# Optimization experiments

Measured on AMD Instinct MI355X. Metric: run time of the kernel, lower is better.

The kernel has to match this reference:

```python
import jax, jax.numpy as jnp
import numpy as np

EMB = 300; H = 150; DEC = 300
VU = 50000; VQ = 30000; VS = 5000
N_COLS = 64; COL_LEN = 6; N_TURNS = 6; IN_LEN = 128; GEN_LEN = 64
MAX_KEEP = 5


def _lstm_cell(x, h, c, Wih, Whh, b):
    z = x @ Wih.T + h @ Whh.T + b
    i, f, g, o = jnp.split(z, 4)
    c = jax.nn.sigmoid(f) * c + jax.nn.sigmoid(i) * jnp.tanh(g)
    h = jax.nn.sigmoid(o) * jnp.tanh(c)
    return h, c


def _run_lstm(xs, Wih, Whh, b):
    hsz = Whh.shape[-1]
    z = jnp.zeros((hsz,), xs.dtype)
    def step(carry, x):
        h, c = _lstm_cell(x, carry[0], carry[1], Wih, Whh, b)
        return (h, c), h
    (h, c), ys = jax.lax.scan(step, (z, z), xs)
    return ys, h, c


def _bilstm(xs, Wih, Whh, b):
    # Wih: [2, 4H, in], Whh: [2, 4H, H], b: [2, 4H]
    yf, hf, cf = _run_lstm(xs, Wih[0], Whh[0], b[0])
    yb, hb, cb = _run_lstm(xs[::-1], Wih[1], Whh[1], b[1])
    return jnp.concatenate([yf, yb[::-1]], -1), jnp.concatenate([hf, hb], -1), jnp.concatenate([cf, cb], -1)


def _attention(q, keys, Wq, Wk, v):
    # Bahdanau: v^T tanh(Wq q + Wk k); context = softmax-weighted sum of keys
    s = jnp.tanh(q @ Wq + keys @ Wk) @ v
    return jax.nn.softmax(s) @ keys


def _forward(utter_emb, query_emb, schema_tok_emb, enc_Wih, enc_Whh, enc_b,
             attn_Wq, attn_Wk, attn_v, dec_Wih0, dec_Whh0, dec_b0,
             dec_Wih1, dec_Whh1, dec_b1, transform_W, sql_W, sql_b, col_W,
             schema_tokens, input_seqs, output_gt):
    attn = lambda k_i, q, keys: _attention(q, keys, attn_Wq[k_i], attn_Wk[k_i], attn_v[k_i])
    # --- schema column encoding: BiLSTM over each column's name tokens ---
    col_tok = schema_tok_emb[schema_tokens]                       # [C, L, EMB]
    _, h, _ = jax.vmap(lambda xs: _bilstm(xs, enc_Wih[0], enc_Whh[0], enc_b[0]))(col_tok)
    schema_embs = h                                               # [C, EMB]
    prev_in, prev_h, prev_c, prev_out = [], [], [], []
    all_dists = []
    bos_emb = query_emb[0]
    for i in range(N_TURNS):
        idx = input_seqs[i]
        # mixed vocab / schema-pointer embedding lookup
        x = jnp.where((idx < VU)[:, None],
                      utter_emb[jnp.clip(idx, 0, VU - 1)],
                      schema_embs[jnp.clip(idx - VU, 0, N_COLS - 1)])
        x, _, _ = _bilstm(x, enc_Wih[1], enc_Whh[1], enc_b[1])    # utter_encoder
        # TextSchemaEncoder (approx): second BiLSTM + schema cross-attention update
        x, fh, fc = _bilstm(x, enc_Wih[2], enc_Whh[2], enc_b[2])
        schema_embs = schema_embs + jax.nn.softmax(schema_embs @ x.T, -1) @ x
        h0, c0 = fh, fc
        if i > 0:
            hist_h = jnp.stack(prev_h); hist_c = jnp.stack(prev_c)
            h0n = h0 + attn(0, h0, hist_h)
            c0 = h0n + attn(0, c0, hist_c)  # replicates original's h-based c init
            h0 = h0n
        prev_in = (prev_in + [x])[:MAX_KEEP]
        prev_h = (prev_h + [fh])[:MAX_KEEP]
        prev_c = (prev_c + [fc])[:MAX_KEEP]
        keys_in = jnp.concatenate(prev_in, 0)
        keys_out = jnp.concatenate(prev_out, 0) if i > 0 else None
        se = schema_embs

        def embed_out(t):
            return jnp.where(t < VQ,
                             query_emb[jnp.clip(t, 0, VQ - 1)],
                             se[jnp.clip(t - VQ, 0, N_COLS - 1)])

        def dec_step(carry, t):
            h1p, c1p, h2p, c2p, dh = carry
            out_emb = embed_out(t)  # teacher forcing
            ctx_s = attn(1, dh, se)
            ctx_i = attn(2, dh, keys_in)
            ctx_o = attn(3, dh, keys_out) if keys_out is not None else jnp.zeros_like(ctx_i)
            ctx = jnp.concatenate([ctx_s, ctx_i, ctx_o])
            xin = jnp.concatenate([out_emb, ctx])                 # [4*EMB]
            h1, c1 = _lstm_cell(xin, h1p, c1p, dec_Wih0, dec_Whh0, dec_b0)
            h2, c2 = _lstm_cell(h1, h2p, c2p, dec_Wih1, dec_Whh1, dec_b1)
            out = jnp.tanh(jnp.concatenate([h2, ctx]) @ transform_W.T)
            score = jnp.concatenate([out @ sql_W.T + sql_b, (out @ col_W.T) @ se.T])
            dist = jax.nn.log_softmax(score)
            am_emb = embed_out(jnp.argmax(dist))
            return (h1, c1, h2, c2, h2), (dist, am_emb)

        init = (h0, c0, h0, c0, h0)
        _, (dists, am_embs) = jax.lax.scan(dec_step, init, output_gt[i, :GEN_LEN - 1])
        prev_out = (prev_out + [jnp.concatenate([bos_emb[None], am_embs], 0)])[:MAX_KEEP]
        all_dists.append(dists)
    return jnp.stack(all_dists, 0)  # [N_TURNS, GEN_LEN-1, VQ+N_COLS]


def setup_inputs() -> dict:
    key = jax.random.key(0)
    ks = jax.random.split(key, 24)
    s = 0.05
    f = lambda k, shape: jax.random.normal(k, shape, jnp.float32) * s
    return {
        "utter_emb": f(ks[0], (VU, EMB)),
        "query_emb": f(ks[1], (VQ, EMB)),
        "schema_tok_emb": f(ks[2], (VS, EMB)),
        "enc_Wih": f(ks[3], (3, 2, 4 * H, EMB)),   # [schema, utter, text-schema] x [fwd, bwd]
        "enc_Whh": f(ks[4], (3, 2, 4 * H, H)),
        "enc_b": f(ks[5], (3, 2, 4 * H)),
        "attn_Wq": f(ks[6], (4, EMB, EMB)),        # [turn, schema, in_tok, out_tok]
        "attn_Wk": f(ks[7], (4, EMB, EMB)),
        "attn_v": f(ks[8], (4, EMB)),
        "dec_Wih0": f(ks[9], (4 * DEC, 4 * EMB)),
        "dec_Whh0": f(ks[10], (4 * DEC, DEC)),
        "dec_b0": f(ks[11], (4 * DEC,)),
        "dec_Wih1": f(ks[12], (4 * DEC, DEC)),
        "dec_Whh1": f(ks[13], (4 * DEC, DEC)),
        "dec_b1": f(ks[14], (4 * DEC,)),
        "transform_W": f(ks[15], (EMB, 4 * EMB)),
        "sql_W": f(ks[16], (VQ, EMB)),
        "sql_b": f(ks[17], (VQ,)),
        "col_W": f(ks[18], (EMB, EMB)),
        "schema_tokens": jax.random.randint(ks[19], (N_COLS, COL_LEN), 0, VS),
        "input_seqs": jax.random.randint(ks[20], (N_TURNS, IN_LEN), 0, VU + N_COLS),
        "output_gt": jax.random.randint(ks[21], (N_TURNS, GEN_LEN), 0, VQ + N_COLS),
    }


def reference(utter_emb, query_emb, schema_tok_emb, enc_Wih, enc_Whh, enc_b,
              attn_Wq, attn_Wk, attn_v, dec_Wih0, dec_Whh0, dec_b0,
              dec_Wih1, dec_Whh1, dec_b1, transform_W, sql_W, sql_b, col_W,
              schema_tokens, input_seqs, output_gt):
    return _forward(utter_emb, query_emb, schema_tok_emb, enc_Wih, enc_Whh, enc_b,
                    attn_Wq, attn_Wk, attn_v, dec_Wih0, dec_Whh0, dec_b0,
                    dec_Wih1, dec_Whh1, dec_b1, transform_W, sql_W, sql_b, col_W,
                    schema_tokens, input_seqs, output_gt)
```

## Files before the change

### kernel.cpp

```cpp
#include <hip/hip_runtime.h>

#define EMB 300
#define VU 50000
#define VQ 30000
#define NCOLS 64
#define COLLEN 6
#define NTURNS 6
#define INLEN 128
#define TSTEPS 63
#define VOUT 30064
#define MAXK 5
#define NWD 60

__device__ __forceinline__ float sigf(float x){ return 1.0f/(1.0f+__expf(-x)); }
__device__ __forceinline__ float tanhf_(float x){ return 1.0f - 2.0f/(1.0f+__expf(2.0f*x)); }
__device__ __forceinline__ float wsum(float v){
#pragma unroll
  for (int o=32;o;o>>=1) v += __shfl_xor(v,o);
  return v;
}
__device__ __forceinline__ float wmax(float v){
#pragma unroll
  for (int o=32;o;o>>=1) v = fmaxf(v,__shfl_xor(v,o));
  return v;
}

__device__ __forceinline__ void gstore(float* p, float v){
  __hip_atomic_store((int*)p, __float_as_int(v), __ATOMIC_RELAXED, __HIP_MEMORY_SCOPE_AGENT);
}
__device__ __forceinline__ float gload(const float* p){
  return __int_as_float(__hip_atomic_load((const int*)p, __ATOMIC_RELAXED, __HIP_MEMORY_SCOPE_AGENT));
}

__device__ __forceinline__ void garrive(int* flags, int w, int P){
  asm volatile("s_waitcnt vmcnt(0)" ::: "memory");
  __syncthreads();
  if (threadIdx.x == 0)
    __hip_atomic_store(flags + w, P, __ATOMIC_RELAXED, __HIP_MEMORY_SCOPE_AGENT);
}
__device__ __forceinline__ void gwait(const int* flags, int P){
  if (threadIdx.x < 64) {
    int v;
    do {
      v = (threadIdx.x < NWD) ? __hip_atomic_load(flags + threadIdx.x, __ATOMIC_RELAXED, __HIP_MEMORY_SCOPE_AGENT) : P;
    } while (__any(v < P));
  }
  __syncthreads();
}

__global__ void k_init(int* flags){ if (threadIdx.x < 64) flags[threadIdx.x] = 0; }

__global__ void k_transposeB(const float* __restrict__ in, float* __restrict__ out,
                             int R, int C, size_t mstride)
{
  __shared__ float tile[32][33];
  const float* inp = in + (size_t)blockIdx.z*mstride;
  float* outp = out + (size_t)blockIdx.z*mstride;
  const int rb = blockIdx.y*32, cb = blockIdx.x*32;
  const int tx = threadIdx.x & 31, ty = threadIdx.x >> 5;
  for (int k = 0; k < 32; k += 8) {
    int r = rb + ty + k, c = cb + tx;
    if (r < R && c < C) tile[ty+k][tx] = inp[(size_t)r*C + c];
  }
  __syncthreads();
  for (int k = 0; k < 32; k += 8) {
    int c = cb + ty + k, r = rb + tx;
    if (c < C && r < R) outp[(size_t)c*R + r] = tile[tx][ty+k];
  }
}

__global__ void k_schema(const float* __restrict__ temb, const int* __restrict__ stok,
                         const float* __restrict__ Wih, const float* __restrict__ Whh,
                         const float* __restrict__ bb, float* __restrict__ SE0)
{
  const int col = blockIdx.x >> 1, dir = blockIdx.x & 1, tid = threadIdx.x;
  __shared__ float hl[150], cl[150], zl[600];
  if (tid < 150) { hl[tid]=0.f; cl[tid]=0.f; }
  __syncthreads();
  const float* Wi = Wih + (size_t)dir*600*300;
  const float* Wh = Whh + (size_t)dir*600*150;
  const float* bd = bb + dir*600;
  for (int s = 0; s < COLLEN; ++s) {
    const int pos = dir ? (COLLEN-1-s) : s;
    const int tok = stok[col*COLLEN + pos];
    const float* x = temb + (size_t)tok*300;
    for (int g = tid; g < 600; g += 256) {
      float a = bd[g];
      const float* wi = Wi + (size_t)g*300;
      for (int c = 0; c < 300; ++c) a += x[c]*wi[c];
      const float* wh = Wh + (size_t)g*150;
      for (int j = 0; j < 150; ++j) a += hl[j]*wh[j];
      zl[g] = a;
    }
    __syncthreads();
    if (tid < 150) {
      float ii=zl[tid], ff=zl[150+tid], gg=zl[300+tid], oo=zl[450+tid];
      float cn = sigf(ff)*cl[tid] + sigf(ii)*tanhf_(gg);
      cl[tid]=cn; hl[tid]=sigf(oo)*tanhf_(cn);
    }
    __syncthreads();
  }
  if (tid < 150) SE0[(size_t)col*300 + dir*150 + tid] = hl[tid];
}

__global__ void k_gemm_xe(const float* __restrict__ src, const float* __restrict__ SEi,
                          const int* __restrict__ iseq, int mode,
                          const float* __restrict__ WihL, const float* __restrict__ bL,
                          float* __restrict__ Xg)
{
  const int g = blockIdx.x*256 + threadIdx.x;
  if (g >= 1200) return;
  const int p0 = blockIdx.y*16;
  const float* xr[16];
#pragma unroll
  for (int t = 0; t < 16; ++t) {
    int p = p0 + t;
    if (mode) xr[t] = src + (size_t)p*300;
    else {
      int tok = iseq[p];
      xr[t] = (tok < VU) ? src + (size_t)tok*300 : SEi + (size_t)(tok - VU)*300;
    }
  }
  const float b = bL[g];
  const float* w = WihL + (size_t)g*300;
  float acc[16];
#pragma unroll
  for (int t = 0; t < 16; ++t) acc[t] = b;
  for (int c = 0; c < 300; ++c) {
    float wv = w[c];
#pragma unroll
    for (int t = 0; t < 16; ++t) acc[t] += wv * xr[t][c];
  }
#pragma unroll
  for (int t = 0; t < 16; ++t) Xg[(size_t)(p0+t)*1200 + g] = acc[t];
}

__global__ __launch_bounds__(640) void k_rec(
    const float* __restrict__ Xg, const float* __restrict__ WhhTL,
    float* __restrict__ ys, float* __restrict__ fh, float* __restrict__ fc)
{
  const int dir = blockIdx.x, tid = threadIdx.x;
  __shared__ __align__(16) float hl[152];
  __shared__ float cl[152], zl[600];
  float w[150];
  const float* wt = WhhTL + (size_t)dir*150*600;
  if (tid < 600) {
#pragma unroll
    for (int j = 0; j < 150; ++j) w[j] = wt[(size_t)j*600 + tid];
  }
  if (tid < 152) { hl[tid] = 0.f; cl[tid] = 0.f; }
  __syncthreads();
  for (int s = 0; s < INLEN; ++s) {
    const int pos = dir ? (INLEN-1-s) : s;
    if (tid < 600) {
      float acc = Xg[(size_t)pos*1200 + dir*600 + tid];
      const float4* h4 = (const float4*)hl;
#pragma unroll
      for (int j4 = 0; j4 < 37; ++j4) {
        float4 h = h4[j4];
        acc += w[4*j4]*h.x + w[4*j4+1]*h.y + w[4*j4+2]*h.z + w[4*j4+3]*h.w;
      }
      acc += w[148]*hl[148] + w[149]*hl[149];
      zl[tid] = acc;
    }
    __syncthreads();
    if (tid < 150) {
      float ii=zl[tid], ff=zl[150+tid], gg=zl[300+tid], oo=zl[450+tid];
      float cn = sigf(ff)*cl[tid] + sigf(ii)*tanhf_(gg);
      cl[tid] = cn;
      float hn = sigf(oo)*tanhf_(cn);
      hl[tid] = hn;
      ys[(size_t)pos*300 + dir*150 + tid] = hn;
    }
    __syncthreads();
  }
  if (tid < 150) { fh[dir*150 + tid] = hl[tid]; fc[dir*150 + tid] = cl[tid]; }
}

__global__ void k_schema_upd(const float* __restrict__ SEi, const float* __restrict__ ys2,
                             float* __restrict__ SEo)
{
  const int row = blockIdx.x, tid = threadIdx.x;
  __shared__ float sl[300], al[128], red[4];
  for (int d = tid; d < 300; d += 256) sl[d] = SEi[(size_t)row*300 + d];
  __syncthreads();
  if (tid < 128) {
    float a = 0;
    const float* yr = ys2 + (size_t)tid*300;
    for (int d = 0; d < 300; ++d) a += sl[d]*yr[d];
    al[tid] = a;
  }
  __syncthreads();
  if (tid < 64) { float m = fmaxf(al[tid], al[tid+64]); m = wmax(m); if (tid==0) red[0]=m; }
  __syncthreads();
  if (tid < 128) al[tid] = __expf(al[tid] - red[0]);
  __syncthreads();
  if (tid < 64) { float s = al[tid] + al[tid+64]; s = wsum(s); if (tid==0) red[1]=s; }
  __syncthreads();
  const float invz = 1.0f/red[1];
  for (int d = tid; d < 300; d += 256) {
    float a = sl[d];
    for (int j = 0; j < 128; ++j) a += (al[j]*invz) * ys2[(size_t)j*300 + d];
    SEo[(size_t)row*300 + d] = a;
  }
}

__global__ void k_hist(const float* __restrict__ fh, const float* __restrict__ fc,
                       const float* __restrict__ ys2,
                       float* __restrict__ HH, float* __restrict__ CH,
                       float* __restrict__ XH, int turn)
{
  const int tid = threadIdx.x;
  for (int i = blockIdx.x*256 + tid; i < INLEN*300; i += 60*256)
    XH[(size_t)turn*INLEN*300 + i] = ys2[i];
  if (blockIdx.x == 0)
    for (int d = tid; d < 300; d += 256) { HH[turn*300+d] = fh[d]; CH[turn*300+d] = fc[d]; }
}

__device__ __forceinline__ const float* key_ptr(int j, int nin, const float* SE1,
                                                const float* XH, const float* OH, int* fam)
{
  if (j < 64) { *fam = 0; return SE1 + (size_t)j*300; }
  if (j < 64+nin) { *fam = 1; return XH + (size_t)(j-64)*300; }
  *fam = 2; return OH + (size_t)(j-64-nin)*300;
}

__global__ void k_tables(const float* __restrict__ SE1, const float* __restrict__ XH,
                         const float* __restrict__ OH, const float* __restrict__ Wk,
                         const float* __restrict__ Wih0, const float* __restrict__ b0,
                         const float* __restrict__ tW, const float* __restrict__ qemb,
                         const int* __restrict__ gt,
                         float* __restrict__ KW, float* __restrict__ G1K,
                         float* __restrict__ G2K, float* __restrict__ Ew,
                         int nin, int nout)
{
  const int NK = 64 + nin + nout;
  const int b = blockIdx.x;
  if (b < NK) {
    int fam; const float* Kr = key_ptr(b, nin, SE1, XH, OH, &fam);
    const float* W = Wk + (size_t)(1+fam)*90000;
    for (int c = threadIdx.x; c < 300; c += 256) {
      float a = 0;
      for (int d = 0; d < 300; ++d) a += Kr[d]*W[(size_t)d*300 + c];
      KW[(size_t)b*300 + c] = a;
    }
  } else if (b < 2*NK) {
    int j = b - NK;
    int fam; const float* Kr = key_ptr(j, nin, SE1, XH, OH, &fam);
    const int cb = 300 + fam*300;
    for (int r = threadIdx.x; r < 1200; r += 256) {
      float a = 0;
      const float* wp = Wih0 + (size_t)r*1200 + cb;
      for (int c = 0; c < 300; ++c) a += Kr[c]*wp[c];
      G1K[(size_t)j*1200 + r] = a;
    }
  } else if (b < 3*NK) {
    int j = b - 2*NK;
    int fam; const float* Kr = key_ptr(j, nin, SE1, XH, OH, &fam);
    const int cb = 300 + fam*300;
    for (int r = threadIdx.x; r < 300; r += 256) {
      float a = 0;
      const float* wp = tW + (size_t)r*1200 + cb;
      for (int c = 0; c < 300; ++c) a += Kr[c]*wp[c];
      G2K[(size_t)j*300 + r] = a;
    }
  } else {
    int t = b - 3*NK;
    int tok = gt[t];
    const float* e = (tok < VQ) ? qemb + (size_t)tok*300 : SE1 + (size_t)(tok-VQ)*300;
    for (int r = threadIdx.x; r < 1200; r += 256) {
      float a = b0[r];
      const float* wp = Wih0 + (size_t)r*1200;
      for (int c = 0; c < 300; ++c) a += e[c]*wp[c];
      Ew[(size_t)t*1200 + r] = a;
    }
  }
}

__global__ __launch_bounds__(256, 1) void k_dec(
    const float* __restrict__ KW, const float* __restrict__ G1KT,
    const float* __restrict__ Ew, const float* __restrict__ WqT,
    const float* __restrict__ av, const float* __restrict__ Wq0,
    const float* __restrict__ Wk0,
    const float* __restrict__ Whh0, const float* __restrict__ Wih1,
    const float* __restrict__ Whh1, const float* __restrict__ b1,
    const float* __restrict__ fh, const float* __restrict__ fc,
    const float* __restrict__ HH, const float* __restrict__ CH,
    float* __restrict__ h0b, float* __restrict__ c0b,
    float* __restrict__ h1b, float* __restrict__ h2b,
    float* __restrict__ qWb, float* __restrict__ scb,
    float* __restrict__ Alog, float* __restrict__ H2log,
    int nin, int nout, int turn, int* __restrict__ flags)
{
  const int NK = 64 + nin + nout;
  const int w = blockIdx.x, tid = threadIdx.x;
  const int wv = tid >> 6, ln = tid & 63;
  __shared__ float g1kl[20][1024];
  __shared__ float kwl[18][320];
  __shared__ float qWlp[3][320];
  __shared__ float vllp[3][320];
  __shared__ float ewl[63][20];
  __shared__ float scl[1024];
  __shared__ float dhl[320], h1l[320];
  __shared__ float pre1[20], pre2[20], zl[20], c1l[5], c2l[5];
  __shared__ float redA[4], alscA[8];
  __shared__ float wr0[4], wr1[4], wr2[4], rm[3], rz[3];
  int P = turn * 253;

  for (int i = tid; i < 20*1024; i += 256) {
    int o = i >> 10, j = i & 1023;
    int row = w*5 + (o % 5) + 300*(o / 5);
    g1kl[o][j] = (j < NK) ? G1KT[(size_t)row*NK + j] : 0.f;
  }
  for (int i = tid; i < 18*320; i += 256) {
    int jo = i / 320, c = i - jo*320;
    int j = w*18 + jo;
    kwl[jo][c] = (c < 300 && j < NK) ? KW[(size_t)j*300 + c] : 0.f;
  }
  for (int i = tid; i < 3*320; i += 256) {
    int f = i / 320, c = i - f*320;
    vllp[f][c] = (c < 300) ? av[300 + f*300 + c] : 0.f;
    qWlp[f][c] = 0.f;
  }
  for (int i = tid; i < 63*20; i += 256) {
    int t = i / 20, o = i - t*20;
    int row = w*5 + (o % 5) + 300*(o / 5);
    ewl[t][o] = Ew[(size_t)t*1200 + row];
  }
  if (tid < 20) { dhl[300+tid] = 0.f; h1l[300+tid] = 0.f; }

  float rwh0[5][5], rwh1[5][5], rwi1[5][5], rwq4[4][5], b1r[5];
#pragma unroll
  for (int r = 0; r < 5; ++r) {
    int row = w*5 + r + 300*wv;
    b1r[r] = b1[row];
#pragma unroll
    for (int k = 0; k < 5; ++k) {
      int d = ln + 64*k;
      rwh0[r][k] = (d < 300) ? Whh0[(size_t)row*300 + d] : 0.f;
      rwh1[r][k] = (d < 300) ? Whh1[(size_t)row*300 + d] : 0.f;
      rwi1[r][k] = (d < 300) ? Wih1[(size_t)row*300 + d] : 0.f;
    }
  }
#pragma unroll
  for (int r = 0; r < 4; ++r) {
    int o = r*4 + wv;
    int q = w*15 + ((o < 15) ? o : 0);
    int fam = q / 300, c = q - fam*300;
    const float* bp = WqT + ((size_t)(1+fam)*300 + c)*300;
#pragma unroll
    for (int k = 0; k < 5; ++k) {
      int d = ln + 64*k;
      rwq4[r][k] = (o < 15 && d < 300) ? bp[d] : 0.f;
    }
  }
  __syncthreads();

  if (w == 0) {
    if (turn == 0) {
      for (int d = tid; d < 300; d += 256) { gstore(h0b+d, fh[d]); gstore(c0b+d, fc[d]); }
    } else {
      const int nh = turn;
      for (int d = tid; d < 300; d += 256) dhl[d] = fh[d];
      __syncthreads();
      for (int rep = 0; rep < 2; ++rep) {
        const float* keys = rep ? CH : HH;
        for (int c = tid; c < 300; c += 256) {
          float a = 0;
          for (int d = 0; d < 300; ++d) a += dhl[d]*Wq0[(size_t)d*300 + c];
          h1l[c] = a;
        }
        __syncthreads();
        for (int k = 0; k < nh; ++k) {
          const float* Kr = keys + (size_t)k*300;
          float part = 0;
          for (int c = tid; c < 300; c += 256) {
            float kw = 0;
            for (int d = 0; d < 300; ++d) kw += Kr[d]*Wk0[(size_t)d*300 + c];
            part += av[c]*tanhf_(h1l[c] + kw);
          }
          part = wsum(part);
          if (ln == 0) redA[wv] = part;
          __syncthreads();
          if (tid == 0) alscA[k] = redA[0]+redA[1]+redA[2]+redA[3];
          __syncthreads();
        }
        if (tid == 0) {
          float m = -1e30f;
          for (int k = 0; k < nh; ++k) m = fmaxf(m, alscA[k]);
          float z = 0;
          for (int k = 0; k < nh; ++k) { alscA[k] = __expf(alscA[k]-m); z += alscA[k]; }
          for (int k = 0; k < nh; ++k) alscA[k] /= z;
        }
        __syncthreads();
        if (rep == 0) {
          for (int c = tid; c < 300; c += 256) {
            float a = dhl[c];
            for (int k = 0; k < nh; ++k) a += alscA[k]*keys[(size_t)k*300 + c];
            scl[c] = a; gstore(h0b+c, a);
          }
          __syncthreads();
          for (int d = tid; d < 300; d += 256) dhl[d] = fc[d];
          __syncthreads();
        } else {
          for (int c = tid; c < 300; c += 256) {
            float a = scl[c];
            for (int k = 0; k < nh; ++k) a += alscA[k]*keys[(size_t)k*300 + c];
            gstore(c0b+c, a);
          }
        }
      }
    }
  }
  garrive(flags, w, ++P);
  gwait(flags, P);

  for (int i = tid; i < 300; i += 256) { float v = gload(h0b+i); dhl[i] = v; h1l[i] = v; }
  if (tid < 5) { float v = gload(c0b + w*5 + tid); c1l[tid] = v; c2l[tid] = v; }
  __syncthreads();

  for (int t = 0; t < TSTEPS; ++t) {
    if (t) {
      for (int i = tid; i < 300; i += 256) dhl[i] = gload(h2b+i);
      __syncthreads();
    }
#pragma unroll
    for (int r = 0; r < 4; ++r) {
      float a = 0;
#pragma unroll
      for (int k = 0; k < 5; ++k) a += rwq4[r][k]*dhl[ln + 64*k];
      a = wsum(a);
      int o = r*4 + wv;
      if (ln == 0 && o < 15) gstore(qWb + w*15 + o, a);
    }
#pragma unroll
    for (int r = 0; r < 5; ++r) {
      float a1 = 0, a2 = 0;
#pragma unroll
      for (int k = 0; k < 5; ++k) {
        float hv = h1l[ln + 64*k], dv = dhl[ln + 64*k];
        a1 += rwh0[r][k]*hv; a2 += rwh1[r][k]*dv;
      }
      a1 = wsum(a1); a2 = wsum(a2);
      if (ln == 0) { pre1[wv*5+r] = a1; pre2[wv*5+r] = a2 + b1r[r]; }
    }
    garrive(flags, w, ++P); gwait(flags, P);

    for (int i = tid; i < 900; i += 256) {
      int f = i / 300, c = i - f*300;
      qWlp[f][c] = gload(qWb + i);
    }
    __syncthreads();
#pragma unroll
    for (int r = 0; r < 5; ++r) {
      int jo = wv*5 + r;
      int j = w*18 + jo;
      bool va = (jo < 18) && (j < NK);
      int f = va ? ((j < 64) ? 0 : (j < 64+nin ? 1 : 2)) : 0;
      int jc = (jo < 18) ? jo : 0;
      float a = 0;
#pragma unroll
      for (int k = 0; k < 5; ++k) {
        int c = ln + 64*k;
        a += vllp[f][c] * tanhf_(qWlp[f][c] + kwl[jc][c]);
      }
      a = wsum(a);
      if (ln == 0 && va) gstore(scb + j, a);
    }
    garrive(flags, w, ++P); gwait(flags, P);

    for (int i = tid; i < NK; i += 256) scl[i] = gload(scb + i);
    __syncthreads();
    {
      float m0=-1e30f, m1=-1e30f, m2=-1e30f;
      for (int j = tid; j < NK; j += 256) {
        float x = scl[j];
        if (j < 64) m0 = fmaxf(m0,x); else if (j < 64+nin) m1 = fmaxf(m1,x); else m2 = fmaxf(m2,x);
      }
      m0 = wmax(m0); m1 = wmax(m1); m2 = wmax(m2);
      if (ln==0){ wr0[wv]=m0; wr1[wv]=m1; wr2[wv]=m2; }
      __syncthreads();
      if (tid==0){
        rm[0]=fmaxf(fmaxf(wr0[0],wr0[1]),fmaxf(wr0[2],wr0[3]));
        rm[1]=fmaxf(fmaxf(wr1[0],wr1[1]),fmaxf(wr1[2],wr1[3]));
        rm[2]=fmaxf(fmaxf(wr2[0],wr2[1]),fmaxf(wr2[2],wr2[3]));
      }
      __syncthreads();
      float s0=0,s1=0,s2=0;
      for (int j = tid; j < NK; j += 256) {
        int f = (j<64)?0:(j<64+nin?1:2);
        float e = __expf(scl[j] - rm[f]);
        scl[j] = e;
        if (f==0) s0+=e; else if (f==1) s1+=e; else s2+=e;
      }
      s0=wsum(s0); s1=wsum(s1); s2=wsum(s2);
      if (ln==0){ wr0[wv]=s0; wr1[wv]=s1; wr2[wv]=s2; }
      __syncthreads();
      if (tid==0){
        rz[0]=wr0[0]+wr0[1]+wr0[2]+wr0[3];
        rz[1]=wr1[0]+wr1[1]+wr1[2]+wr1[3];
        rz[2]=wr2[0]+wr2[1]+wr2[2]+wr2[3];
      }
      __syncthreads();
      for (int j = tid; j < NK; j += 256) {
        int f = (j<64)?0:(j<64+nin?1:2);
        scl[j] /= rz[f];
      }
      __syncthreads();
    }
    if (tid < 18) { int j = w*18 + tid; if (j < NK) Alog[(size_t)t*1024 + j] = scl[j]; }
    {
      const int KC = NK >> 6;
#pragma unroll 1
      for (int r = 0; r < 5; ++r) {
        int o = wv*5 + r;
        float a = 0;
        for (int k = 0; k < KC; ++k) { int j = ln + 64*k; a += scl[j]*g1kl[o][j]; }
        a = wsum(a);
        if (ln == 0) zl[o] = a + ewl[t][o] + pre1[o];
      }
    }
    __syncthreads();
    if (tid < 5) {
      float ii=zl[tid], ff=zl[5+tid], gg=zl[10+tid], oo=zl[15+tid];
      float cn = sigf(ff)*c1l[tid] + sigf(ii)*tanhf_(gg);
      c1l[tid] = cn;
      gstore(h1b + w*5 + tid, sigf(oo)*tanhf_(cn));
    }
    garrive(flags, w, ++P); gwait(flags, P);

    for (int i = tid; i < 300; i += 256) h1l[i] = gload(h1b + i);
    __syncthreads();
#pragma unroll
    for (int r = 0; r < 5; ++r) {
      float a = 0;
#pragma unroll
      for (int k = 0; k < 5; ++k) a += rwi1[r][k]*h1l[ln + 64*k];
      a = wsum(a);
      if (ln == 0) zl[wv*5+r] = a + pre2[wv*5+r];
    }
    __syncthreads();
    if (tid < 5) {
      int d = w*5 + tid;
      float ii=zl[tid], ff=zl[5+tid], gg=zl[10+tid], oo=zl[15+tid];
      float cn = sigf(ff)*c2l[tid] + sigf(ii)*tanhf_(gg);
      c2l[tid] = cn;
      float hn = sigf(oo)*tanhf_(cn);
      gstore(h2b + d, hn);
      H2log[(size_t)t*300 + d] = hn;
    }
    garrive(flags, w, ++P); gwait(flags, P);
  }
}

__global__ void k_ctxout2(const float* __restrict__ H2, const float* __restrict__ Al,
                          const float* __restrict__ G2K, const float* __restrict__ tW,
                          const float* __restrict__ colW,
                          float* __restrict__ o63, float* __restrict__ t63, int NK)
{
  const int t = blockIdx.x, tid = threadIdx.x;
  __shared__ float ol[304], h2l[304];
  for (int d = tid; d < 300; d += 256) h2l[d] = H2[(size_t)t*300 + d];
  __syncthreads();
  for (int r = tid; r < 300; r += 256) {
    float a = 0;
    const float* tr = tW + (size_t)r*1200;
    for (int d = 0; d < 300; ++d) a += h2l[d]*tr[d];
    for (int j = 0; j < NK; ++j) a += Al[(size_t)t*1024 + j]*G2K[(size_t)j*300 + r];
    float v = tanhf_(a);
    ol[r] = v;
    o63[(size_t)t*300 + r] = v;
  }
  __syncthreads();
  for (int e = tid; e < 300; e += 256) {
    float a = 0;
    const float* wc = colW + (size_t)e*300;
    for (int d = 0; d < 300; ++d) a += ol[d]*wc[d];
    t63[(size_t)t*300 + e] = a;
  }
}

__global__ void k_score(const float* __restrict__ o63, const float* __restrict__ t63,
                        const float* __restrict__ sqlW, const float* __restrict__ sqlb,
                        const float* __restrict__ SE1, float* __restrict__ Dout)
{
  const int v = blockIdx.x*256 + threadIdx.x;
  if (v >= VOUT) return;
  const int t0 = blockIdx.y*16;
  const int tn = (t0 + 16 <= 63) ? 16 : (63 - t0);
  float acc[16];
#pragma unroll
  for (int k = 0; k < 16; ++k) acc[k] = 0.f;
  if (v < VQ) {
    const float* w = sqlW + (size_t)v*300;
    for (int d = 0; d < 300; ++d) {
      float wv_ = w[d];
#pragma unroll
      for (int k = 0; k < 16; ++k) acc[k] += wv_ * o63[(size_t)(t0+k)*300 + d];
    }
    float b = sqlb[v];
    for (int k = 0; k < tn; ++k) Dout[(size_t)(t0+k)*VOUT + v] = acc[k] + b;
  } else {
    const float* w = SE1 + (size_t)(v - VQ)*300;
    for (int d = 0; d < 300; ++d) {
      float wv_ = w[d];
#pragma unroll
      for (int k = 0; k < 16; ++k) acc[k] += wv_ * t63[(size_t)(t0+k)*300 + d];
    }
    for (int k = 0; k < tn; ++k) Dout[(size_t)(t0+k)*VOUT + v] = acc[k];
  }
}

__global__ void k_lsm(float* __restrict__ rows, int* __restrict__ amx)
{
  const int t = blockIdx.x, tid = threadIdx.x, wv = tid>>6, ln = tid&63;
  float* row = rows + (size_t)t*VOUT;
  __shared__ float rv[4], rs[4];
  __shared__ int ri[4];
  float m = -1e30f; int mi = VOUT;
  for (int j = tid; j < VOUT; j += 256) {
    float x = row[j];
    if (x > m) { m = x; mi = j; }
  }
#pragma unroll
  for (int o = 32; o; o >>= 1) {
    float om = __shfl_xor(m, o); int oi = __shfl_xor(mi, o);
    if (om > m || (om == m && oi < mi)) { m = om; mi = oi; }
  }
  if (ln == 0) { rv[wv] = m; ri[wv] = mi; }
  __syncthreads();
  if (tid == 0) {
    for (int k = 1; k < 4; ++k)
      if (rv[k] > rv[0] || (rv[k] == rv[0] && ri[k] < ri[0])) { rv[0]=rv[k]; ri[0]=ri[k]; }
    amx[t] = ri[0];
  }
  __syncthreads();
  const float M = rv[0];
  float s = 0;
  for (int j = tid; j < VOUT; j += 256) s += __expf(row[j] - M);
  s = wsum(s);
  if (ln == 0) rs[wv] = s;
  __syncthreads();
  const float L = M + logf(rs[0]+rs[1]+rs[2]+rs[3]);
  for (int j = tid; j < VOUT; j += 256) row[j] -= L;
}

__global__ void k_amemb(const int* __restrict__ amx, const float* __restrict__ qemb,
                        const float* __restrict__ SE1, float* __restrict__ OHt)
{
  for (int i = threadIdx.x; i < 64*300; i += 256) {
    int r = i/300, d = i - r*300;
    const float* src;
    if (r == 0) src = qemb;
    else {
      int id = amx[r-1];
      src = (id < VQ) ? qemb + (size_t)id*300 : SE1 + (size_t)(id-VQ)*300;
    }
    OHt[i] = src[d];
  }
}

extern "C" void kernel_launch(void* const* d_in, const int* in_sizes, int n_in,
                              void* d_out, int out_size, void* d_ws, size_t ws_size,
                              hipStream_t stream)
{
  const float* utter = (const float*)d_in[0];
  const float* qemb  = (const float*)d_in[1];
  const float* temb  = (const float*)d_in[2];
  const float* eWih  = (const float*)d_in[3];
  const float* eWhh  = (const float*)d_in[4];
  const float* eb    = (const float*)d_in[5];
  const float* aWq   = (const float*)d_in[6];
  const float* aWk   = (const float*)d_in[7];
  const float* av    = (const float*)d_in[8];
  const float* dWih0 = (const float*)d_in[9];
  const float* dWhh0 = (const float*)d_in[10];
  const float* db0   = (const float*)d_in[11];
  const float* dWih1 = (const float*)d_in[12];
  const float* dWhh1 = (const float*)d_in[13];
  const float* db1   = (const float*)d_in[14];
  const float* tW    = (const float*)d_in[15];
  const float* sqlW  = (const float*)d_in[16];
  const float* sqlb  = (const float*)d_in[17];
  const float* colW  = (const float*)d_in[18];
  const int* stok    = (const int*)d_in[19];
  const int* iseq    = (const int*)d_in[20];
  const int* ogt     = (const int*)d_in[21];
  float* dout = (float*)d_out;

  float* base = (float*)d_ws;
  size_t off = 0;
  auto A = [&](size_t n)->float*{ float* r = base + off; off += (n + 63) & ~(size_t)63; return r; };
  float* SE   = A(7*64*300);
  float* XH   = A(5*128*300);
  float* OH   = A(5*64*300);
  float* HH   = A(5*300);
  float* CH   = A(5*300);
  float* ys1  = A(128*300);
  float* ys2  = A(128*300);
  float* Xg   = A(128*1200);
  float* fh   = A(320);
  float* fc   = A(320);
  float* fhs  = A(320);
  float* fcs  = A(320);
  float* h0b  = A(320);
  float* c0b  = A(320);
  float* h1b  = A(320);
  float* h2b  = A(320);
  float* qWb  = A(960);
  float* scb  = A(1024);
  float* KW   = A(1024*300);
  float* G1K  = A(1024*1200);
  float* G1KT = A(1200*1024);
  float* G2K  = A(1024*300);
  float* EwB  = A(63*1200);
  float* Alog = A(63*1024);
  float* H2lg = A(64*300);
  float* o63  = A(64*300);
  float* t63  = A(64*300);
  A(512);
  float* WqT  = A(4*300*300);
  float* WhhT = A(6*150*600);
  int* amx   = (int*)A(64);
  int* flags = (int*)A(64);
  (void)ws_size; (void)in_sizes; (void)n_in; (void)out_size;

  dim3 B256(256);
  k_init<<<1, 64, 0, stream>>>(flags);
  k_transposeB<<<dim3(10,10,4), B256, 0, stream>>>(aWq, WqT, 300, 300, 90000);
  k_transposeB<<<dim3(5,19,6), B256, 0, stream>>>(eWhh, WhhT, 600, 150, 90000);
  k_schema<<<128, B256, 0, stream>>>(temb, stok, eWih, eWhh, eb, SE);

  for (int i = 0; i < NTURNS; ++i) {
    const int kin  = (i+1 < MAXK) ? (i+1) : MAXK;
    const int kout = (i < MAXK) ? i : MAXK;
    const int nin = kin*128, nout = kout*64;
    const int NK = 64 + nin + nout;
    float* SEi = SE + (size_t)i*19200;
    float* SEo = SE + (size_t)(i+1)*19200;

    k_gemm_xe<<<dim3(5,8), B256, 0, stream>>>(utter, SEi, iseq + i*INLEN, 0,
                                              eWih + 360000, eb + 1200, Xg);
    k_rec<<<2, 640, 0, stream>>>(Xg, WhhT + 180000, ys1, fhs, fcs);
    k_gemm_xe<<<dim3(5,8), B256, 0, stream>>>(ys1, SEi, iseq + i*INLEN, 1,
                                              eWih + 720000, eb + 2400, Xg);
    k_rec<<<2, 640, 0, stream>>>(Xg, WhhT + 360000, ys2, fh, fc);
    k_schema_upd<<<64, B256, 0, stream>>>(SEi, ys2, SEo);
    if (i < MAXK)
      k_hist<<<60, B256, 0, stream>>>(fh, fc, ys2, HH, CH, XH, i);
    k_tables<<<3*NK + 63, B256, 0, stream>>>(SEo, XH, OH, aWk, dWih0, db0, tW, qemb,
                                             ogt + i*64, KW, G1K, G2K, EwB, nin, nout);
    k_transposeB<<<dim3(38, (NK+31)/32, 1), B256, 0, stream>>>(G1K, G1KT, NK, 1200, 0);
    k_dec<<<NWD, B256, 0, stream>>>(KW, G1KT, EwB, WqT, av, aWq, aWk,
                                    dWhh0, dWih1, dWhh1, db1, fh, fc, HH, CH,
                                    h0b, c0b, h1b, h2b, qWb, scb, Alog, H2lg,
                                    nin, nout, i, flags);
    k_ctxout2<<<63, B256, 0, stream>>>(H2lg, Alog, G2K, tW, colW, o63, t63, NK);
    k_score<<<dim3(118,4), B256, 0, stream>>>(o63, t63, sqlW, sqlb, SEo, dout + (size_t)i*63*VOUT);
    k_lsm<<<63, B256, 0, stream>>>(dout + (size_t)i*63*VOUT, amx);
    if (i < MAXK)
      k_amemb<<<1, B256, 0, stream>>>(amx, qemb, SEo, OH + (size_t)i*19200);
  }
}
```

Before: 18.69 ms.

## Transpose weights for coalesced reads, fuse small kernels, pad sync flags, overlap decoder barriers

Adds one-time transposes of Wih0, tW and encoder Wih so that the GEMV-style loops in k_gemm_xe, k_tables and k_ctxout2 read weights coalesced across threads. k_tables now writes G1K already transposed, which removes a per-turn transpose kernel. k_hist is folded into k_schema_upd and k_amemb into k_lsm, cutting launches. The grid-barrier flags are padded onto separate cache lines, and in k_dec the barrier arrives earlier so independent work overlaps the spin-wait, with only the needed qW slices loaded. k_rec prefetches the next Xg row and splits its accumulation across several partial sums to shorten the dependency chain.

```diff
diff --git a/kernel.cpp b/kernel.cpp
--- a/kernel.cpp
+++ b/kernel.cpp
@@ -11,6 +11,7 @@
 #define VOUT 30064
 #define MAXK 5
 #define NWD 60
+#define FPAD 32
 
 __device__ __forceinline__ float sigf(float x){ return 1.0f/(1.0f+__expf(-x)); }
 __device__ __forceinline__ float tanhf_(float x){ return 1.0f - 2.0f/(1.0f+__expf(2.0f*x)); }
@@ -36,19 +37,21 @@
   asm volatile("s_waitcnt vmcnt(0)" ::: "memory");
   __syncthreads();
   if (threadIdx.x == 0)
-    __hip_atomic_store(flags + w, P, __ATOMIC_RELAXED, __HIP_MEMORY_SCOPE_AGENT);
+    __hip_atomic_store(flags + w*FPAD, P, __ATOMIC_RELAXED, __HIP_MEMORY_SCOPE_AGENT);
 }
 __device__ __forceinline__ void gwait(const int* flags, int P){
   if (threadIdx.x < 64) {
     int v;
     do {
-      v = (threadIdx.x < NWD) ? __hip_atomic_load(flags + threadIdx.x, __ATOMIC_RELAXED, __HIP_MEMORY_SCOPE_AGENT) : P;
+      v = (threadIdx.x < NWD) ? __hip_atomic_load(flags + threadIdx.x*FPAD, __ATOMIC_RELAXED, __HIP_MEMORY_SCOPE_AGENT) : P;
     } while (__any(v < P));
   }
   __syncthreads();
 }
 
-__global__ void k_init(int* flags){ if (threadIdx.x < 64) flags[threadIdx.x] = 0; }
+__global__ void k_init(int* flags){
+  for (int i = threadIdx.x; i < NWD*FPAD; i += 256) flags[i] = 0;
+}
 
 __global__ void k_transposeB(const float* __restrict__ in, float* __restrict__ out,
                              int R, int C, size_t mstride)
@@ -105,7 +108,7 @@
 
 __global__ void k_gemm_xe(const float* __restrict__ src, const float* __restrict__ SEi,
                           const int* __restrict__ iseq, int mode,
-                          const float* __restrict__ WihL, const float* __restrict__ bL,
+                          const float* __restrict__ WihT, const float* __restrict__ bL,
                           float* __restrict__ Xg)
 {
   const int g = blockIdx.x*256 + threadIdx.x;
@@ -122,12 +125,11 @@
     }
   }
   const float b = bL[g];
-  const float* w = WihL + (size_t)g*300;
   float acc[16];
 #pragma unroll
   for (int t = 0; t < 16; ++t) acc[t] = b;
   for (int c = 0; c < 300; ++c) {
-    float wv = w[c];
+    float wv = WihT[(size_t)c*1200 + g];
 #pragma unroll
     for (int t = 0; t < 16; ++t) acc[t] += wv * xr[t][c];
   }
@@ -150,18 +152,23 @@
   }
   if (tid < 152) { hl[tid] = 0.f; cl[tid] = 0.f; }
   __syncthreads();
+  float xg = (tid < 600) ? Xg[(size_t)(dir ? INLEN-1 : 0)*1200 + dir*600 + tid] : 0.f;
   for (int s = 0; s < INLEN; ++s) {
     const int pos = dir ? (INLEN-1-s) : s;
+    const int nxt = dir ? (INLEN-2-s) : (s+1);
+    float xg_nx = (s+1 < INLEN && tid < 600) ? Xg[(size_t)nxt*1200 + dir*600 + tid] : 0.f;
     if (tid < 600) {
-      float acc = Xg[(size_t)pos*1200 + dir*600 + tid];
+      float aa[8];
+#pragma unroll
+      for (int q = 0; q < 8; ++q) aa[q] = 0.f;
       const float4* h4 = (const float4*)hl;
 #pragma unroll
       for (int j4 = 0; j4 < 37; ++j4) {
         float4 h = h4[j4];
-        acc += w[4*j4]*h.x + w[4*j4+1]*h.y + w[4*j4+2]*h.z + w[4*j4+3]*h.w;
-      }
-      acc += w[148]*hl[148] + w[149]*hl[149];
-      zl[tid] = acc;
+        aa[j4&7] += w[4*j4]*h.x + w[4*j4+1]*h.y + w[4*j4+2]*h.z + w[4*j4+3]*h.w;
+      }
+      zl[tid] = xg + ((aa[0]+aa[1])+(aa[2]+aa[3])) + ((aa[4]+aa[5])+(aa[6]+aa[7]))
+                + w[148]*hl[148] + w[149]*hl[149];
     }
     __syncthreads();
     if (tid < 150) {
@@ -173,12 +180,16 @@
       ys[(size_t)pos*300 + dir*150 + tid] = hn;
     }
     __syncthreads();
+    xg = xg_nx;
   }
   if (tid < 150) { fh[dir*150 + tid] = hl[tid]; fc[dir*150 + tid] = cl[tid]; }
 }
 
 __global__ void k_schema_upd(const float* __restrict__ SEi, const float* __restrict__ ys2,
-                             float* __restrict__ SEo)
+                             float* __restrict__ SEo,
+                             const float* __restrict__ fh, const float* __restrict__ fc,
+                             float* __restrict__ HH, float* __restrict__ CH,
+                             float* __restrict__ XH, int turn)
 {
   const int row = blockIdx.x, tid = threadIdx.x;
   __shared__ float sl[300], al[128], red[4];
@@ -203,18 +214,12 @@
     for (int j = 0; j < 128; ++j) a += (al[j]*invz) * ys2[(size_t)j*300 + d];
     SEo[(size_t)row*300 + d] = a;
   }
-}
-
-__global__ void k_hist(const float* __restrict__ fh, const float* __restrict__ fc,
-                       const float* __restrict__ ys2,
-                       float* __restrict__ HH, float* __restrict__ CH,
-                       float* __restrict__ XH, int turn)
-{
-  const int tid = threadIdx.x;
-  for (int i = blockIdx.x*256 + tid; i < INLEN*300; i += 60*256)
-    XH[(size_t)turn*INLEN*300 + i] = ys2[i];
-  if (blockIdx.x == 0)
-    for (int d = tid; d < 300; d += 256) { HH[turn*300+d] = fh[d]; CH[turn*300+d] = fc[d]; }
+  if (turn < MAXK) {
+    for (int i = row*600 + tid; i < row*600 + 600; i += 256)
+      XH[(size_t)turn*INLEN*300 + i] = ys2[i];
+    if (row == 0)
+      for (int d = tid; d < 300; d += 256) { HH[turn*300+d] = fh[d]; CH[turn*300+d] = fc[d]; }
+  }
 }
 
 __device__ __forceinline__ const float* key_ptr(int j, int nin, const float* SE1,
@@ -227,10 +232,10 @@
 
 __global__ void k_tables(const float* __restrict__ SE1, const float* __restrict__ XH,
                          const float* __restrict__ OH, const float* __restrict__ Wk,
-                         const float* __restrict__ Wih0, const float* __restrict__ b0,
-                         const float* __restrict__ tW, const float* __restrict__ qemb,
+                         const float* __restrict__ Wih0T, const float* __restrict__ b0,
+                         const float* __restrict__ tWT, const float* __restrict__ qemb,
                          const int* __restrict__ gt,
-                         float* __restrict__ KW, float* __restrict__ G1K,
+                         float* __restrict__ KW, float* __restrict__ G1KT,
                          float* __restrict__ G2K, float* __restrict__ Ew,
                          int nin, int nout)
 {
@@ -250,9 +255,8 @@
     const int cb = 300 + fam*300;
     for (int r = threadIdx.x; r < 1200; r += 256) {
       float a = 0;
-      const float* wp = Wih0 + (size_t)r*1200 + cb;
-      for (int c = 0; c < 300; ++c) a += Kr[c]*wp[c];
-      G1K[(size_t)j*1200 + r] = a;
+      for (int c = 0; c < 300; ++c) a += Kr[c]*Wih0T[(size_t)(cb+c)*1200 + r];
+      G1KT[(size_t)r*NK + j] = a;
     }
   } else if (b < 3*NK) {
     int j = b - 2*NK;
@@ -260,8 +264,7 @@
     const int cb = 300 + fam*300;
     for (int r = threadIdx.x; r < 300; r += 256) {
       float a = 0;
-      const float* wp = tW + (size_t)r*1200 + cb;
-      for (int c = 0; c < 300; ++c) a += Kr[c]*wp[c];
+      for (int c = 0; c < 300; ++c) a += Kr[c]*tWT[(size_t)(cb+c)*300 + r];
       G2K[(size_t)j*300 + r] = a;
     }
   } else {
@@ -270,8 +273,7 @@
     const float* e = (tok < VQ) ? qemb + (size_t)tok*300 : SE1 + (size_t)(tok-VQ)*300;
     for (int r = threadIdx.x; r < 1200; r += 256) {
       float a = b0[r];
-      const float* wp = Wih0 + (size_t)r*1200;
-      for (int c = 0; c < 300; ++c) a += e[c]*wp[c];
+      for (int c = 0; c < 300; ++c) a += e[c]*Wih0T[(size_t)c*1200 + r];
       Ew[(size_t)t*1200 + r] = a;
     }
   }
@@ -354,6 +356,10 @@
       rwq4[r][k] = (o < 15 && d < 300) ? bp[d] : 0.f;
     }
   }
+  const int jlo = (w*18 < NK) ? w*18 : NK-1;
+  const int jhi = (w*18+17 < NK) ? w*18+17 : NK-1;
+  const int f0 = (jlo < 64) ? 0 : (jlo < 64+nin ? 1 : 2);
+  const int f1 = (jhi < 64) ? 0 : (jhi < 64+nin ? 1 : 2);
   __syncthreads();
 
   if (w == 0) {
@@ -433,6 +439,7 @@
       int o = r*4 + wv;
       if (ln == 0 && o < 15) gstore(qWb + w*15 + o, a);
     }
+    garrive(flags, w, ++P);
 #pragma unroll
     for (int r = 0; r < 5; ++r) {
       float a1 = 0, a2 = 0;
@@ -444,9 +451,9 @@
       a1 = wsum(a1); a2 = wsum(a2);
       if (ln == 0) { pre1[wv*5+r] = a1; pre2[wv*5+r] = a2 + b1r[r]; }
     }
-    garrive(flags, w, ++P); gwait(flags, P);
-
-    for (int i = tid; i < 900; i += 256) {
+    gwait(flags, P);
+
+    for (int i = f0*300 + tid; i < (f1+1)*300; i += 256) {
       int f = i / 300, c = i - f*300;
       qWlp[f][c] = gload(qWb + i);
     }
@@ -467,7 +474,8 @@
       a = wsum(a);
       if (ln == 0 && va) gstore(scb + j, a);
     }
-    garrive(flags, w, ++P); gwait(flags, P);
+    garrive(flags, w, ++P);
+    gwait(flags, P);
 
     for (int i = tid; i < NK; i += 256) scl[i] = gload(scb + i);
     __syncthreads();
@@ -508,7 +516,6 @@
       }
       __syncthreads();
     }
-    if (tid < 18) { int j = w*18 + tid; if (j < NK) Alog[(size_t)t*1024 + j] = scl[j]; }
     {
       const int KC = NK >> 6;
 #pragma unroll 1
@@ -527,7 +534,9 @@
       c1l[tid] = cn;
       gstore(h1b + w*5 + tid, sigf(oo)*tanhf_(cn));
     }
-    garrive(flags, w, ++P); gwait(flags, P);
+    garrive(flags, w, ++P);
+    if (tid < 18) { int j = w*18 + tid; if (j < NK) Alog[(size_t)t*1024 + j] = scl[j]; }
+    gwait(flags, P);
 
     for (int i = tid; i < 300; i += 256) h1l[i] = gload(h1b + i);
     __syncthreads();
@@ -540,21 +549,22 @@
       if (ln == 0) zl[wv*5+r] = a + pre2[wv*5+r];
     }
     __syncthreads();
+    float hn = 0.f;
     if (tid < 5) {
-      int d = w*5 + tid;
       float ii=zl[tid], ff=zl[5+tid], gg=zl[10+tid], oo=zl[15+tid];
       float cn = sigf(ff)*c2l[tid] + sigf(ii)*tanhf_(gg);
       c2l[tid] = cn;
-      float hn = sigf(oo)*tanhf_(cn);
-      gstore(h2b + d, hn);
-      H2log[(size_t)t*300 + d] = hn;
-    }
-    garrive(flags, w, ++P); gwait(flags, P);
+      hn = sigf(oo)*tanhf_(cn);
+      gstore(h2b + w*5 + tid, hn);
+    }
+    garrive(flags, w, ++P);
+    if (tid < 5) H2log[(size_t)t*300 + w*5 + tid] = hn;
+    gwait(flags, P);
   }
 }
 
 __global__ void k_ctxout2(const float* __restrict__ H2, const float* __restrict__ Al,
-                          const float* __restrict__ G2K, const float* __restrict__ tW,
+                          const float* __restrict__ G2K, const float* __restrict__ tWT,
                           const float* __restrict__ colW,
                           float* __restrict__ o63, float* __restrict__ t63, int NK)
 {
@@ -564,8 +574,7 @@
   __syncthreads();
   for (int r = tid; r < 300; r += 256) {
     float a = 0;
-    const float* tr = tW + (size_t)r*1200;
-    for (int d = 0; d < 300; ++d) a += h2l[d]*tr[d];
+    for (int d = 0; d < 300; ++d) a += h2l[d]*tWT[(size_t)d*300 + r];
     for (int j = 0; j < NK; ++j) a += Al[(size_t)t*1024 + j]*G2K[(size_t)j*300 + r];
     float v = tanhf_(a);
     ol[r] = v;
@@ -611,7 +620,8 @@
   }
 }
 
-__global__ void k_lsm(float* __restrict__ rows, int* __restrict__ amx)
+__global__ void k_lsm(float* __restrict__ rows, const float* __restrict__ qemb,
+                      const float* __restrict__ SE1, float* __restrict__ OHt)
 {
   const int t = blockIdx.x, tid = threadIdx.x, wv = tid>>6, ln = tid&63;
   float* row = rows + (size_t)t*VOUT;
@@ -632,7 +642,6 @@
   if (tid == 0) {
     for (int k = 1; k < 4; ++k)
       if (rv[k] > rv[0] || (rv[k] == rv[0] && ri[k] < ri[0])) { rv[0]=rv[k]; ri[0]=ri[k]; }
-    amx[t] = ri[0];
   }
   __syncthreads();
   const float M = rv[0];
@@ -643,20 +652,13 @@
   __syncthreads();
   const float L = M + logf(rs[0]+rs[1]+rs[2]+rs[3]);
   for (int j = tid; j < VOUT; j += 256) row[j] -= L;
-}
-
-__global__ void k_amemb(const int* __restrict__ amx, const float* __restrict__ qemb,
-                        const float* __restrict__ SE1, float* __restrict__ OHt)
-{
-  for (int i = threadIdx.x; i < 64*300; i += 256) {
-    int r = i/300, d = i - r*300;
-    const float* src;
-    if (r == 0) src = qemb;
-    else {
-      int id = amx[r-1];
-      src = (id < VQ) ? qemb + (size_t)id*300 : SE1 + (size_t)(id-VQ)*300;
-    }
-    OHt[i] = src[d];
+  if (OHt) {
+    int id = ri[0];
+    const float* src = (id < VQ) ? qemb + (size_t)id*300 : SE1 + (size_t)(id-VQ)*300;
+    for (int d = tid; d < 300; d += 256) {
+      OHt[(size_t)(t+1)*300 + d] = src[d];
+      if (t == 0) OHt[d] = qemb[d];
+    }
   }
 }
 
@@ -691,44 +693,48 @@
   float* base = (float*)d_ws;
   size_t off = 0;
   auto A = [&](size_t n)->float*{ float* r = base + off; off += (n + 63) & ~(size_t)63; return r; };
-  float* SE   = A(7*64*300);
-  float* XH   = A(5*128*300);
-  float* OH   = A(5*64*300);
-  float* HH   = A(5*300);
-  float* CH   = A(5*300);
-  float* ys1  = A(128*300);
-  float* ys2  = A(128*300);
-  float* Xg   = A(128*1200);
-  float* fh   = A(320);
-  float* fc   = A(320);
-  float* fhs  = A(320);
-  float* fcs  = A(320);
-  float* h0b  = A(320);
-  float* c0b  = A(320);
-  float* h1b  = A(320);
-  float* h2b  = A(320);
-  float* qWb  = A(960);
-  float* scb  = A(1024);
-  float* KW   = A(1024*300);
-  float* G1K  = A(1024*1200);
-  float* G1KT = A(1200*1024);
-  float* G2K  = A(1024*300);
-  float* EwB  = A(63*1200);
-  float* Alog = A(63*1024);
-  float* H2lg = A(64*300);
-  float* o63  = A(64*300);
-  float* t63  = A(64*300);
+  float* SE    = A(7*64*300);
+  float* XH    = A(5*128*300);
+  float* OH    = A(5*64*300);
+  float* HH    = A(5*300);
+  float* CH    = A(5*300);
+  float* ys1   = A(128*300);
+  float* ys2   = A(128*300);
+  float* Xg    = A(128*1200);
+  float* fh    = A(320);
+  float* fc    = A(320);
+  float* fhs   = A(320);
+  float* fcs   = A(320);
+  float* h0b   = A(320);
+  float* c0b   = A(320);
+  float* h1b   = A(320);
+  float* h2b   = A(320);
+  float* qWb   = A(960);
+  float* scb   = A(1024);
+  float* KW    = A(1024*300);
+  float* G1KT  = A(1200*1024);
+  float* G2K   = A(1024*300);
+  float* EwB   = A(63*1200);
+  float* Alog  = A(63*1024);
+  float* H2lg  = A(64*300);
+  float* o63   = A(64*300);
+  float* t63   = A(64*300);
   A(512);
-  float* WqT  = A(4*300*300);
-  float* WhhT = A(6*150*600);
-  int* amx   = (int*)A(64);
-  int* flags = (int*)A(64);
+  float* WqT   = A(4*300*300);
+  float* WhhT  = A(6*150*600);
+  float* Wih0T = A(1200*1200);
+  float* tWT   = A(1200*300);
+  float* eWT   = A(2*300*1200);
+  int* flags = (int*)A(NWD*FPAD);
   (void)ws_size; (void)in_sizes; (void)n_in; (void)out_size;
 
   dim3 B256(256);
-  k_init<<<1, 64, 0, stream>>>(flags);
+  k_init<<<1, B256, 0, stream>>>(flags);
   k_transposeB<<<dim3(10,10,4), B256, 0, stream>>>(aWq, WqT, 300, 300, 90000);
   k_transposeB<<<dim3(5,19,6), B256, 0, stream>>>(eWhh, WhhT, 600, 150, 90000);
+  k_transposeB<<<dim3(38,38,1), B256, 0, stream>>>(dWih0, Wih0T, 1200, 1200, 0);
+  k_transposeB<<<dim3(38,10,1), B256, 0, stream>>>(tW, tWT, 300, 1200, 0);
+  k_transposeB<<<dim3(10,38,2), B256, 0, stream>>>(eWih + 360000, eWT, 1200, 300, 360000);
   k_schema<<<128, B256, 0, stream>>>(temb, stok, eWih, eWhh, eb, SE);
 
   for (int i = 0; i < NTURNS; ++i) {
@@ -740,25 +746,21 @@
     float* SEo = SE + (size_t)(i+1)*19200;
 
     k_gemm_xe<<<dim3(5,8), B256, 0, stream>>>(utter, SEi, iseq + i*INLEN, 0,
-                                              eWih + 360000, eb + 1200, Xg);
+                                              eWT, eb + 1200, Xg);
     k_rec<<<2, 640, 0, stream>>>(Xg, WhhT + 180000, ys1, fhs, fcs);
     k_gemm_xe<<<dim3(5,8), B256, 0, stream>>>(ys1, SEi, iseq + i*INLEN, 1,
-                                              eWih + 720000, eb + 2400, Xg);
+                                              eWT + 360000, eb + 2400, Xg);
     k_rec<<<2, 640, 0, stream>>>(Xg, WhhT + 360000, ys2, fh, fc);
-    k_schema_upd<<<64, B256, 0, stream>>>(SEi, ys2, SEo);
-    if (i < MAXK)
-      k_hist<<<60, B256, 0, stream>>>(fh, fc, ys2, HH, CH, XH, i);
-    k_tables<<<3*NK + 63, B256, 0, stream>>>(SEo, XH, OH, aWk, dWih0, db0, tW, qemb,
-                                             ogt + i*64, KW, G1K, G2K, EwB, nin, nout);
-    k_transposeB<<<dim3(38, (NK+31)/32, 1), B256, 0, stream>>>(G1K, G1KT, NK, 1200, 0);
+    k_schema_upd<<<64, B256, 0, stream>>>(SEi, ys2, SEo, fh, fc, HH, CH, XH, i);
+    k_tables<<<3*NK + 63, B256, 0, stream>>>(SEo, XH, OH, aWk, Wih0T, db0, tWT, qemb,
+                                             ogt + i*64, KW, G1KT, G2K, EwB, nin, nout);
     k_dec<<<NWD, B256, 0, stream>>>(KW, G1KT, EwB, WqT, av, aWq, aWk,
                                     dWhh0, dWih1, dWhh1, db1, fh, fc, HH, CH,
                                     h0b, c0b, h1b, h2b, qWb, scb, Alog, H2lg,
                                     nin, nout, i, flags);
-    k_ctxout2<<<63, B256, 0, stream>>>(H2lg, Alog, G2K, tW, colW, o63, t63, NK);
+    k_ctxout2<<<63, B256, 0, stream>>>(H2lg, Alog, G2K, tWT, colW, o63, t63, NK);
     k_score<<<dim3(118,4), B256, 0, stream>>>(o63, t63, sqlW, sqlb, SEo, dout + (size_t)i*63*VOUT);
-    k_lsm<<<63, B256, 0, stream>>>(dout + (size_t)i*63*VOUT, amx);
-    if (i < MAXK)
-      k_amemb<<<1, B256, 0, stream>>>(amx, qemb, SEo, OH + (size_t)i*19200);
-  }
-}
+    k_lsm<<<63, B256, 0, stream>>>(dout + (size_t)i*63*VOUT, qemb, SEo,
+                                   (i < MAXK) ? OH + (size_t)i*19200 : nullptr);
+  }
+}
```

Result: slower. 19.33 ms (+3.4%).
